# Kernel tuning notes

Hardware: AMD Instinct MI355X
Metric: run time of the kernel (lower is better)

## Reference

```python
import jax, jax.numpy as jnp
import numpy as np

A = 1000          # nr_assets
LQ = 2048         # len_quote
C = 3             # channels == nr_in
H = 10            # sub_net_out (LSTM hidden)
NLAYER = 3        # hidden_l
HID = A * H       # 10000
MID = HID // 2    # 5000
NPOS = A + 1      # 1001
NOUT = 2001       # nr_out


def lstm_step0(x, w_ih, b_ih, b_hh):
    # One LSTM cell step from zero (h0, c0). w_hh @ h0 == 0 so w_hh drops out
    # of the forward math (it still exists as a parameter). torch gate order i,f,g,o.
    gates = x @ w_ih.T + b_ih + b_hh            # [A, 4H]
    i, f, g, o = jnp.split(gates, 4, axis=-1)
    c = jax.nn.sigmoid(i) * jnp.tanh(g)          # f*c0 == 0
    return jax.nn.sigmoid(o) * jnp.tanh(c)       # [A, H]


def setup_inputs() -> dict:
    key = jax.random.key(0)
    ks = jax.random.split(key, 20)
    s = 0.1
    inp = {
        "quotes": jax.random.normal(ks[0], (A, LQ, C), dtype=jnp.float32),
        "position": jax.random.normal(ks[1], (NPOS,), dtype=jnp.float32),
        # LSTM layer 0 (input C), layers 1,2 (input H)
        "w_ih_l0": s * jax.random.normal(ks[2], (4 * H, C), dtype=jnp.float32),
        "w_hh_l0": s * jax.random.normal(ks[3], (4 * H, H), dtype=jnp.float32),
        "b_ih_l0": s * jax.random.normal(ks[4], (4 * H,), dtype=jnp.float32),
        "b_hh_l0": s * jax.random.normal(ks[5], (4 * H,), dtype=jnp.float32),
        "w_ih_l1": s * jax.random.normal(ks[6], (4 * H, H), dtype=jnp.float32),
        "w_hh_l1": s * jax.random.normal(ks[7], (4 * H, H), dtype=jnp.float32),
        "b_ih_l1": s * jax.random.normal(ks[8], (4 * H,), dtype=jnp.float32),
        "b_hh_l1": s * jax.random.normal(ks[9], (4 * H,), dtype=jnp.float32),
        "w_ih_l2": s * jax.random.normal(ks[10], (4 * H, H), dtype=jnp.float32),
        "w_hh_l2": s * jax.random.normal(ks[11], (4 * H, H), dtype=jnp.float32),
        "b_ih_l2": s * jax.random.normal(ks[12], (4 * H,), dtype=jnp.float32),
        "b_hh_l2": s * jax.random.normal(ks[13], (4 * H,), dtype=jnp.float32),
        "w1": s * jax.random.normal(ks[14], (MID, HID), dtype=jnp.float32),
        "b1": s * jax.random.normal(ks[15], (MID,), dtype=jnp.float32),
        "w2": s * jax.random.normal(ks[16], (NOUT, MID + NPOS), dtype=jnp.float32),
        "b2": s * jax.random.normal(ks[17], (NOUT,), dtype=jnp.float32),
    }
    return inp


def reference(quotes, position,
              w_ih_l0, w_hh_l0, b_ih_l0, b_hh_l0,
              w_ih_l1, w_hh_l1, b_ih_l1, b_hh_l1,
              w_ih_l2, w_hh_l2, b_ih_l2, b_hh_l2,
              w1, b1, w2, b2):
    # Original loop: per-asset quote.view(1, len_quote, C) -> seq_len-1 LSTM with
    # batch=len_quote from zero state; out[:, -1] keeps only the last time row.
    # Equivalent batched form: one 3-layer LSTM cell step on quotes[:, -1, :].
    x = quotes[:, -1, :]                          # [A, C]
    h = lstm_step0(x, w_ih_l0, b_ih_l0, b_hh_l0)  # [A, H]
    h = lstm_step0(h, w_ih_l1, b_ih_l1, b_hh_l1)
    h = lstm_step0(h, w_ih_l2, b_ih_l2, b_hh_l2)
    h = jnp.tanh(h)
    conc = h.reshape(1, -1)                       # concat of [1,H] per asset == [1, A*H]
    lin = jnp.tanh(conc @ w1.T + b1)              # [1, MID]
    out_pos = jnp.concatenate([lin, position.reshape(1, -1)], axis=1)
    return out_pos @ w2.T + b2                    # [1, NOUT]
```

## Files before the change

kernel.cpp:

```cpp
#include <hip/hip_runtime.h>
#include <math.h>

#define A_N    1000
#define LQ_N   2048
#define C_N    3
#define H_N    10
#define HID_N  10000
#define MID_N  5000
#define NPOS_N 1001
#define NOUT_N 2001
#define W2COLS 6001
#define VCAT_N 6004

__device__ __forceinline__ float sigmoidf_(float x) { return 1.0f / (1.0f + expf(-x)); }

__device__ __forceinline__ float wave_reduce(float acc) {
    #pragma unroll
    for (int off = 32; off > 0; off >>= 1) acc += __shfl_down(acc, off, 64);
    return acc;
}

__global__ void __launch_bounds__(256) lstm_head(
    const float* __restrict__ quotes,
    const float* __restrict__ wih0, const float* __restrict__ bih0, const float* __restrict__ bhh0,
    const float* __restrict__ wih1, const float* __restrict__ bih1, const float* __restrict__ bhh1,
    const float* __restrict__ wih2, const float* __restrict__ bih2, const float* __restrict__ bhh2,
    const float* __restrict__ pos,
    float* __restrict__ conc, float* __restrict__ vcat)
{
    if (blockIdx.x == 4) {
        for (int j = threadIdx.x; j < NPOS_N; j += 256)
            vcat[MID_N + j] = pos[j];
        if (threadIdx.x < 3) vcat[W2COLS + threadIdx.x] = 0.0f;
        return;
    }

    int a = blockIdx.x * blockDim.x + threadIdx.x;
    if (a >= A_N) return;

    const float* q = quotes + (size_t)a * LQ_N * C_N + (size_t)(LQ_N - 1) * C_N;
    float x0 = q[0], x1 = q[1], x2 = q[2];

    float g[40];
    float h[H_N];

    #pragma unroll
    for (int j = 0; j < 40; ++j)
        g[j] = x0 * wih0[j * 3 + 0] + x1 * wih0[j * 3 + 1] + x2 * wih0[j * 3 + 2]
             + bih0[j] + bhh0[j];
    #pragma unroll
    for (int k = 0; k < H_N; ++k) {
        float cc = sigmoidf_(g[k]) * tanhf(g[20 + k]);
        h[k] = sigmoidf_(g[30 + k]) * tanhf(cc);
    }

    #pragma unroll
    for (int j = 0; j < 40; ++j) {
        float s = bih1[j] + bhh1[j];
        #pragma unroll
        for (int k = 0; k < H_N; ++k) s += h[k] * wih1[j * 10 + k];
        g[j] = s;
    }
    float h2[H_N];
    #pragma unroll
    for (int k = 0; k < H_N; ++k) {
        float cc = sigmoidf_(g[k]) * tanhf(g[20 + k]);
        h2[k] = sigmoidf_(g[30 + k]) * tanhf(cc);
    }

    #pragma unroll
    for (int j = 0; j < 40; ++j) {
        float s = bih2[j] + bhh2[j];
        #pragma unroll
        for (int k = 0; k < H_N; ++k) s += h2[k] * wih2[j * 10 + k];
        g[j] = s;
    }
    #pragma unroll
    for (int k = 0; k < H_N; ++k) {
        float cc = sigmoidf_(g[k]) * tanhf(g[20 + k]);
        float hh = sigmoidf_(g[30 + k]) * tanhf(cc);
        conc[a * H_N + k] = tanhf(hh);
    }
}

__global__ void __launch_bounds__(256) mv1(
    const float* __restrict__ w1, const float* __restrict__ b1,
    const float* __restrict__ conc, float* __restrict__ vcat)
{
    int lane = threadIdx.x & 63;
    int wid  = threadIdx.x >> 6;
    int row  = blockIdx.x * 4 + wid;

    const float4* rb = reinterpret_cast<const float4*>(w1 + (size_t)row * HID_N);
    const float4* cv = reinterpret_cast<const float4*>(conc);

    float acc0 = 0.f, acc1 = 0.f, acc2 = 0.f, acc3 = 0.f;
    int i = lane;
    #pragma unroll 1
    for (int k = 0; k < 9; ++k, i += 256) {
        float4 a0 = rb[i];       float4 a1 = rb[i + 64];
        float4 a2 = rb[i + 128]; float4 a3 = rb[i + 192];
        float4 c0 = cv[i];       float4 c1 = cv[i + 64];
        float4 c2 = cv[i + 128]; float4 c3 = cv[i + 192];
        acc0 += a0.x * c0.x + a0.y * c0.y + a0.z * c0.z + a0.w * c0.w;
        acc1 += a1.x * c1.x + a1.y * c1.y + a1.z * c1.z + a1.w * c1.w;
        acc2 += a2.x * c2.x + a2.y * c2.y + a2.z * c2.z + a2.w * c2.w;
        acc3 += a3.x * c3.x + a3.y * c3.y + a3.z * c3.z + a3.w * c3.w;
    }
    {
        float4 a0 = rb[i];       float4 a1 = rb[i + 64];  float4 a2 = rb[i + 128];
        float4 c0 = cv[i];       float4 c1 = cv[i + 64];  float4 c2 = cv[i + 128];
        acc0 += a0.x * c0.x + a0.y * c0.y + a0.z * c0.z + a0.w * c0.w;
        acc1 += a1.x * c1.x + a1.y * c1.y + a1.z * c1.z + a1.w * c1.w;
        acc2 += a2.x * c2.x + a2.y * c2.y + a2.z * c2.z + a2.w * c2.w;
    }
    if (lane < 4) {
        float4 a = rb[2496 + lane];
        float4 c = cv[2496 + lane];
        acc3 += a.x * c.x + a.y * c.y + a.z * c.z + a.w * c.w;
    }

    float acc = wave_reduce((acc0 + acc1) + (acc2 + acc3));
    if (lane == 0) vcat[row] = tanhf(acc + b1[row]);
}

__global__ void __launch_bounds__(256) mv2(
    const float* __restrict__ w2, const float* __restrict__ b2,
    const float* __restrict__ vcat, float* __restrict__ out)
{
    int lane = threadIdx.x & 63;
    int wid  = threadIdx.x >> 6;
    int row  = blockIdx.x * 4 + wid;
    if (row >= NOUT_N) return;

    const float* wr = w2 + (size_t)row * W2COLS;
    const int p    = (4 - (row & 3)) & 3;
    const int n    = W2COLS - p;
    const int n4   = n >> 2;
    const int tail = n & 3;

    float acc0 = 0.f, acc1 = 0.f, acc2 = 0.f, acc3 = 0.f;
    if (lane < p) acc0 += wr[lane] * vcat[lane];

    const float4* rb = reinterpret_cast<const float4*>(wr + p);
    int i = lane;
    #pragma unroll 1
    for (; i + 192 < n4; i += 256) {
        float4 a0 = rb[i];       float4 a1 = rb[i + 64];
        float4 a2 = rb[i + 128]; float4 a3 = rb[i + 192];
        int j0 = p + 4 * i, j1 = j0 + 256, j2 = j0 + 512, j3 = j0 + 768;
        acc0 += a0.x * vcat[j0] + a0.y * vcat[j0+1] + a0.z * vcat[j0+2] + a0.w * vcat[j0+3];
        acc1 += a1.x * vcat[j1] + a1.y * vcat[j1+1] + a1.z * vcat[j1+2] + a1.w * vcat[j1+3];
        acc2 += a2.x * vcat[j2] + a2.y * vcat[j2+1] + a2.z * vcat[j2+2] + a2.w * vcat[j2+3];
        acc3 += a3.x * vcat[j3] + a3.y * vcat[j3+1] + a3.z * vcat[j3+2] + a3.w * vcat[j3+3];
    }
    #pragma unroll 1
    for (; i < n4; i += 64) {
        float4 a = rb[i];
        int j = p + 4 * i;
        acc0 += a.x * vcat[j] + a.y * vcat[j+1] + a.z * vcat[j+2] + a.w * vcat[j+3];
    }
    if (lane < tail) {
        int j = p + 4 * n4 + lane;
        acc0 += wr[j] * vcat[j];
    }

    float s = wave_reduce((acc0 + acc1) + (acc2 + acc3));
    if (lane == 0) out[row] = s + b2[row];
}

extern "C" void kernel_launch(void* const* d_in, const int* in_sizes, int n_in,
                              void* d_out, int out_size, void* d_ws, size_t ws_size,
                              hipStream_t stream)
{
    const float* quotes = (const float*)d_in[0];
    const float* pos    = (const float*)d_in[1];
    const float* wih0   = (const float*)d_in[2];
    const float* bih0   = (const float*)d_in[4];
    const float* bhh0   = (const float*)d_in[5];
    const float* wih1   = (const float*)d_in[6];
    const float* bih1   = (const float*)d_in[8];
    const float* bhh1   = (const float*)d_in[9];
    const float* wih2   = (const float*)d_in[10];
    const float* bih2   = (const float*)d_in[12];
    const float* bhh2   = (const float*)d_in[13];
    const float* w1     = (const float*)d_in[14];
    const float* b1     = (const float*)d_in[15];
    const float* w2     = (const float*)d_in[16];
    const float* b2     = (const float*)d_in[17];
    float* out = (float*)d_out;

    float* vcat = (float*)d_ws;
    float* conc = vcat + 6016;

    lstm_head<<<5, 256, 0, stream>>>(
        quotes, wih0, bih0, bhh0, wih1, bih1, bhh1, wih2, bih2, bhh2,
        pos, conc, vcat);

    mv1<<<MID_N / 4, 256, 0, stream>>>(w1, b1, conc, vcat);

    mv2<<<(NOUT_N + 3) / 4, 256, 0, stream>>>(w2, b2, vcat, out);
}
```

Measured before the change: 64.83 us.

## Fuse both matvecs into one persistent kernel with grid barriers

Replaces the separate mv1 and mv2 launches with a single persistent kernel of 1024 blocks that uses a two-level atomic grid barrier. The first matvec is split into quarter-row tasks whose partial sums are reduced and passed through tanh after the barrier, and the second matvec runs after another barrier. The aim is to remove a launch boundary and balance the w1 work across all waves. In exchange it adds a memset launch and barrier spin overhead, and it relies on all 1024 blocks being co-resident, which risks deadlock if occupancy is insufficient.

New measurement: 239.9 us. +270.0%, slower.

```diff
diff --git a/kernel.cpp b/kernel.cpp
--- a/kernel.cpp
+++ b/kernel.cpp
@@ -10,14 +10,43 @@
 #define NPOS_N 1001
 #define NOUT_N 2001
 #define W2COLS 6001
-#define VCAT_N 6004
+
+#define NBLK   1024
+#define NWAVE  (NBLK * 4)
+#define NTASKA 20000
+#define QF4    625
+#define ROWF4  2500
+
+#define WS_CONC    0
+#define WS_VCAT    10000
+#define WS_PARTIAL 16016
+#define WS_BARRIER 36016
 
 __device__ __forceinline__ float sigmoidf_(float x) { return 1.0f / (1.0f + expf(-x)); }
-
+__device__ __forceinline__ float dot4(float4 a, float4 b) {
+    return a.x * b.x + a.y * b.y + a.z * b.z + a.w * b.w;
+}
 __device__ __forceinline__ float wave_reduce(float acc) {
     #pragma unroll
     for (int off = 32; off > 0; off >>= 1) acc += __shfl_down(acc, off, 64);
     return acc;
+}
+
+__device__ __forceinline__ void grid_barrier(unsigned* bar, int phase) {
+    unsigned* sub    = bar + phase * 32;
+    unsigned* master = sub + 16;
+    __syncthreads();
+    if (threadIdx.x == 0) {
+        __threadfence();
+        unsigned old = __hip_atomic_fetch_add(&sub[blockIdx.x & 15], 1u,
+                                              __ATOMIC_ACQ_REL, __HIP_MEMORY_SCOPE_AGENT);
+        if (old == (NBLK / 16) - 1)
+            __hip_atomic_fetch_add(master, 1u, __ATOMIC_ACQ_REL, __HIP_MEMORY_SCOPE_AGENT);
+        while (__hip_atomic_load(master, __ATOMIC_ACQUIRE, __HIP_MEMORY_SCOPE_AGENT) < 16u)
+            __builtin_amdgcn_s_sleep(2);
+        __threadfence();
+    }
+    __syncthreads();
 }
 
 __global__ void __launch_bounds__(256) lstm_head(
@@ -83,90 +112,92 @@
     }
 }
 
-__global__ void __launch_bounds__(256) mv1(
+__global__ void __launch_bounds__(256, 4) fused_mv(
     const float* __restrict__ w1, const float* __restrict__ b1,
-    const float* __restrict__ conc, float* __restrict__ vcat)
+    const float* __restrict__ w2, const float* __restrict__ b2,
+    float* __restrict__ ws, float* __restrict__ out)
 {
-    int lane = threadIdx.x & 63;
-    int wid  = threadIdx.x >> 6;
-    int row  = blockIdx.x * 4 + wid;
-
-    const float4* rb = reinterpret_cast<const float4*>(w1 + (size_t)row * HID_N);
-    const float4* cv = reinterpret_cast<const float4*>(conc);
-
-    float acc0 = 0.f, acc1 = 0.f, acc2 = 0.f, acc3 = 0.f;
-    int i = lane;
-    #pragma unroll 1
-    for (int k = 0; k < 9; ++k, i += 256) {
-        float4 a0 = rb[i];       float4 a1 = rb[i + 64];
-        float4 a2 = rb[i + 128]; float4 a3 = rb[i + 192];
-        float4 c0 = cv[i];       float4 c1 = cv[i + 64];
-        float4 c2 = cv[i + 128]; float4 c3 = cv[i + 192];
-        acc0 += a0.x * c0.x + a0.y * c0.y + a0.z * c0.z + a0.w * c0.w;
-        acc1 += a1.x * c1.x + a1.y * c1.y + a1.z * c1.z + a1.w * c1.w;
-        acc2 += a2.x * c2.x + a2.y * c2.y + a2.z * c2.z + a2.w * c2.w;
-        acc3 += a3.x * c3.x + a3.y * c3.y + a3.z * c3.z + a3.w * c3.w;
-    }
+    float* conc    = ws + WS_CONC;
+    float* vcat    = ws + WS_VCAT;
+    float* partial = ws + WS_PARTIAL;
+    unsigned* bar  = (unsigned*)(ws + WS_BARRIER);
+
+    const int lane = threadIdx.x & 63;
+    const int wid  = threadIdx.x >> 6;
+    const int gw   = blockIdx.x * 4 + wid;
+
     {
-        float4 a0 = rb[i];       float4 a1 = rb[i + 64];  float4 a2 = rb[i + 128];
-        float4 c0 = cv[i];       float4 c1 = cv[i + 64];  float4 c2 = cv[i + 128];
-        acc0 += a0.x * c0.x + a0.y * c0.y + a0.z * c0.z + a0.w * c0.w;
-        acc1 += a1.x * c1.x + a1.y * c1.y + a1.z * c1.z + a1.w * c1.w;
-        acc2 += a2.x * c2.x + a2.y * c2.y + a2.z * c2.z + a2.w * c2.w;
-    }
-    if (lane < 4) {
-        float4 a = rb[2496 + lane];
-        float4 c = cv[2496 + lane];
-        acc3 += a.x * c.x + a.y * c.y + a.z * c.z + a.w * c.w;
-    }
-
-    float acc = wave_reduce((acc0 + acc1) + (acc2 + acc3));
-    if (lane == 0) vcat[row] = tanhf(acc + b1[row]);
-}
-
-__global__ void __launch_bounds__(256) mv2(
-    const float* __restrict__ w2, const float* __restrict__ b2,
-    const float* __restrict__ vcat, float* __restrict__ out)
-{
-    int lane = threadIdx.x & 63;
-    int wid  = threadIdx.x >> 6;
-    int row  = blockIdx.x * 4 + wid;
-    if (row >= NOUT_N) return;
-
-    const float* wr = w2 + (size_t)row * W2COLS;
-    const int p    = (4 - (row & 3)) & 3;
-    const int n    = W2COLS - p;
-    const int n4   = n >> 2;
-    const int tail = n & 3;
-
-    float acc0 = 0.f, acc1 = 0.f, acc2 = 0.f, acc3 = 0.f;
-    if (lane < p) acc0 += wr[lane] * vcat[lane];
-
-    const float4* rb = reinterpret_cast<const float4*>(wr + p);
-    int i = lane;
-    #pragma unroll 1
-    for (; i + 192 < n4; i += 256) {
-        float4 a0 = rb[i];       float4 a1 = rb[i + 64];
-        float4 a2 = rb[i + 128]; float4 a3 = rb[i + 192];
-        int j0 = p + 4 * i, j1 = j0 + 256, j2 = j0 + 512, j3 = j0 + 768;
-        acc0 += a0.x * vcat[j0] + a0.y * vcat[j0+1] + a0.z * vcat[j0+2] + a0.w * vcat[j0+3];
-        acc1 += a1.x * vcat[j1] + a1.y * vcat[j1+1] + a1.z * vcat[j1+2] + a1.w * vcat[j1+3];
-        acc2 += a2.x * vcat[j2] + a2.y * vcat[j2+1] + a2.z * vcat[j2+2] + a2.w * vcat[j2+3];
-        acc3 += a3.x * vcat[j3] + a3.y * vcat[j3+1] + a3.z * vcat[j3+2] + a3.w * vcat[j3+3];
-    }
-    #pragma unroll 1
-    for (; i < n4; i += 64) {
-        float4 a = rb[i];
-        int j = p + 4 * i;
-        acc0 += a.x * vcat[j] + a.y * vcat[j+1] + a.z * vcat[j+2] + a.w * vcat[j+3];
-    }
-    if (lane < tail) {
-        int j = p + 4 * n4 + lane;
-        acc0 += wr[j] * vcat[j];
-    }
-
-    float s = wave_reduce((acc0 + acc1) + (acc2 + acc3));
-    if (lane == 0) out[row] = s + b2[row];
+        const float4* w1v = reinterpret_cast<const float4*>(w1);
+        const float4* cv  = reinterpret_cast<const float4*>(conc);
+        for (int t = gw; t < NTASKA; t += NWAVE) {
+            int row = t >> 2;
+            int cb  = (t & 3) * QF4;
+            int ce  = cb + QF4;
+            const float4* wrow = w1v + (size_t)row * ROWF4;
+            float s0 = 0.f, s1 = 0.f;
+            int c = cb + lane;
+            #pragma unroll 1
+            for (; c + 64 < ce; c += 128) {
+                float4 a0 = wrow[c];      float4 v0 = cv[c];
+                float4 a1 = wrow[c + 64]; float4 v1 = cv[c + 64];
+                s0 += dot4(a0, v0);
+                s1 += dot4(a1, v1);
+            }
+            if (c < ce) s0 += dot4(wrow[c], cv[c]);
+            float s = wave_reduce(s0 + s1);
+            if (lane == 0) partial[t] = s;
+        }
+    }
+
+    grid_barrier(bar, 0);
+
+    {
+        int gtid = blockIdx.x * 256 + threadIdx.x;
+        if (gtid < MID_N) {
+            float4 pp = *reinterpret_cast<const float4*>(partial + 4 * gtid);
+            vcat[gtid] = tanhf(pp.x + pp.y + pp.z + pp.w + b1[gtid]);
+        }
+    }
+
+    grid_barrier(bar, 1);
+
+    if (gw < NOUT_N) {
+        const int row = gw;
+        const float* wr = w2 + (size_t)row * W2COLS;
+        const int p    = (4 - (row & 3)) & 3;
+        const int n    = W2COLS - p;
+        const int n4   = n >> 2;
+        const int tail = n & 3;
+
+        float acc0 = 0.f, acc1 = 0.f, acc2 = 0.f, acc3 = 0.f;
+        if (lane < p) acc0 += wr[lane] * vcat[lane];
+
+        const float4* rb = reinterpret_cast<const float4*>(wr + p);
+        int i = lane;
+        #pragma unroll 1
+        for (; i + 192 < n4; i += 256) {
+            float4 a0 = rb[i];       float4 a1 = rb[i + 64];
+            float4 a2 = rb[i + 128]; float4 a3 = rb[i + 192];
+            int j0 = p + 4 * i, j1 = j0 + 256, j2 = j0 + 512, j3 = j0 + 768;
+            acc0 += a0.x * vcat[j0] + a0.y * vcat[j0+1] + a0.z * vcat[j0+2] + a0.w * vcat[j0+3];
+            acc1 += a1.x * vcat[j1] + a1.y * vcat[j1+1] + a1.z * vcat[j1+2] + a1.w * vcat[j1+3];
+            acc2 += a2.x * vcat[j2] + a2.y * vcat[j2+1] + a2.z * vcat[j2+2] + a2.w * vcat[j2+3];
+            acc3 += a3.x * vcat[j3] + a3.y * vcat[j3+1] + a3.z * vcat[j3+2] + a3.w * vcat[j3+3];
+        }
+        #pragma unroll 1
+        for (; i < n4; i += 64) {
+            float4 a = rb[i];
+            int j = p + 4 * i;
+            acc0 += a.x * vcat[j] + a.y * vcat[j+1] + a.z * vcat[j+2] + a.w * vcat[j+3];
+        }
+        if (lane < tail) {
+            int j = p + 4 * n4 + lane;
+            acc0 += wr[j] * vcat[j];
+        }
+
+        float s = wave_reduce((acc0 + acc1) + (acc2 + acc3));
+        if (lane == 0) out[row] = s + b2[row];
+    }
 }
 
 extern "C" void kernel_launch(void* const* d_in, const int* in_sizes, int n_in,
@@ -190,14 +221,15 @@
     const float* b2     = (const float*)d_in[17];
     float* out = (float*)d_out;
 
-    float* vcat = (float*)d_ws;
-    float* conc = vcat + 6016;
+    float* ws   = (float*)d_ws;
+    float* conc = ws + WS_CONC;
+    float* vcat = ws + WS_VCAT;
+
+    hipMemsetAsync((char*)d_ws + WS_BARRIER * sizeof(float), 0, 256, stream);
 
     lstm_head<<<5, 256, 0, stream>>>(
         quotes, wih0, bih0, bhh0, wih1, bih1, bhh1, wih2, bih2, bhh2,
         pos, conc, vcat);
 
-    mv1<<<MID_N / 4, 256, 0, stream>>>(w1, b1, conc, vcat);
-
-    mv2<<<(NOUT_N + 3) / 4, 256, 0, stream>>>(w2, b2, vcat, out);
-}
+    fused_mv<<<NBLK, 256, 0, stream>>>(w1, b1, w2, b2, ws, out);
+}
```
